# Kernel tuning notes

Hardware: AMD Instinct MI355X
Metric: run time of the kernel (lower is better)

The kernel has to match this reference:

```python
import jax, jax.numpy as jnp
import numpy as np

NUM_QUANTIZERS = 8
CODEBOOK_SIZE = 1024
DIM = 64
B, N = 8, 8192


def setup_inputs() -> dict:
    key = jax.random.key(0)
    kx, kc = jax.random.split(key)
    x = jax.random.normal(kx, (B, N, DIM), dtype=jnp.float32)
    # one codebook per quantizer stage (shared_codebook=False)
    codebooks = jax.random.normal(kc, (NUM_QUANTIZERS, CODEBOOK_SIZE, DIM), dtype=jnp.float32)
    return {"x": x, "codebooks": codebooks}


def reference(x, codebooks):
    """Residual VQ: sequential nearest-codebook lookup with residual subtraction.

    x:         [b, n, d]
    codebooks: [Q, K, d]
    returns quantized_out: [b, n, d]
    """

    def step(carry, cb):
        residual, qout = carry                       # [b,n,d], [b,n,d]
        # squared euclidean distances, [b,n,K]
        r_sq = jnp.sum(residual * residual, axis=-1, keepdims=True)
        c_sq = jnp.sum(cb * cb, axis=-1)             # [K]
        dots = jnp.einsum('bnd,kd->bnk', residual, cb)
        dist = r_sq - 2.0 * dots + c_sq              # [b,n,K]
        idx = jnp.argmin(dist, axis=-1)              # [b,n]
        quant = cb[idx]                              # [b,n,d] gather
        # straight-through estimator (VectorQuantize forward)
        quant_st = residual + jax.lax.stop_gradient(quant - residual)
        new_residual = residual - jax.lax.stop_gradient(quant)
        return (new_residual, qout + quant_st), idx

    init = (x, jnp.zeros_like(x))
    (residual, quantized_out), all_indices = jax.lax.scan(step, init, codebooks)
    return quantized_out
```

## Files before the change

### kernel.cpp

```cpp
#include <hip/hip_runtime.h>

#define NQ 8
#define KCODES 1024
#define D 64
#define CHUNK 64
#define NCHUNK 16
#define TPB 256
#define TOKPB 64
#define BIAS 96.0f

using short8 = __attribute__((ext_vector_type(8))) short;
using f32x4  = __attribute__((ext_vector_type(4))) float;

#define GLOBAL_AS __attribute__((address_space(1)))
#define LDS_AS    __attribute__((address_space(3)))

static __device__ __forceinline__ unsigned bf16_rne_bits(float f) {
    unsigned u = __float_as_uint(f);
    return (u + 0x7fffu + ((u >> 16) & 1u)) >> 16;
}
static __device__ __forceinline__ unsigned umn(unsigned a, unsigned b) { return a < b ? a : b; }
static __device__ __forceinline__ unsigned umx(unsigned a, unsigned b) { return a > b ? a : b; }
static __device__ __forceinline__ unsigned umed3(unsigned a, unsigned b, unsigned c) {
    return umx(umn(a, b), umn(umx(a, b), c));
}

__global__ __launch_bounds__(256) void prep_cb(const float* __restrict__ cb,
                                               int4* __restrict__ ws_cb) {
    int id = blockIdx.x * 256 + threadIdx.x;
    int n_rel = id & 63;
    int plane = (id >> 6) & 15;
    int ch    = (id >> 10) & 15;
    int q     = id >> 14;
    int g = plane & 3, kt = (plane >> 2) & 1, term = plane >> 3;
    int n = ch * CHUNK + n_rel;
    const float* src = cb + ((size_t)(q * KCODES + n)) * D + kt * 32 + g * 8;
    union { short s[8]; int4 v; } u;
    #pragma unroll
    for (int j = 0; j < 8; ++j) {
        float f = -src[j];
        unsigned hb = bf16_rne_bits(f);
        if (term == 0) {
            u.s[j] = (short)hb;
        } else {
            float lo = f - __uint_as_float(hb << 16);
            u.s[j] = (short)bf16_rne_bits(lo);
        }
    }
    ws_cb[id] = u.v;
}

__global__ __launch_bounds__(256) void prep_csq(const float* __restrict__ cb,
                                                float* __restrict__ ws_csq,
                                                float* __restrict__ ws_csqh) {
    int id = blockIdx.x * 256 + threadIdx.x;
    const float* c = cb + (size_t)id * D;
    float s0 = 0.f, s1 = 0.f, s2 = 0.f, s3 = 0.f;
    #pragma unroll
    for (int j = 0; j < 16; ++j) {
        s0 = fmaf(c[4*j+0], c[4*j+0], s0);
        s1 = fmaf(c[4*j+1], c[4*j+1], s1);
        s2 = fmaf(c[4*j+2], c[4*j+2], s2);
        s3 = fmaf(c[4*j+3], c[4*j+3], s3);
    }
    float cs = (s0 + s1) + (s2 + s3);
    ws_csq[id]  = cs;
    ws_csqh[id] = 0.5f * cs + BIAS;
}

__global__ __launch_bounds__(TPB, 4) void rvq_mfma(
    const float* __restrict__ x,
    const float* __restrict__ cb,
    const int4* __restrict__ ws_cb,
    const float* __restrict__ ws_csq,
    float* __restrict__ out)
{
    __shared__ __align__(16) int4  lds_stage[1024];
    __shared__ __align__(16) float lds_resid[TOKPB * 68];
    __shared__ float    lds_csqh[CHUNK];
    __shared__ unsigned lds_cand[2][TOKPB * 3];
    __shared__ int      lds_pick[TOKPB];

    const int tid   = threadIdx.x;
    const int lane  = tid & 63;
    const int wave  = tid >> 6;
    const int group = wave >> 1;
    const int half  = wave & 1;
    const int g     = lane >> 4;
    const int c     = lane & 15;
    const int tok0  = blockIdx.x * TOKPB;

    {
        const int t = tid >> 2, part = tid & 3;
        const float4* xp = (const float4*)(x + (size_t)(tok0 + t) * D + part * 16);
        float4* rr = (float4*)(lds_resid + t * 68 + part * 16);
        #pragma unroll
        for (int k2 = 0; k2 < 4; ++k2) rr[k2] = xp[k2];
    }

    const char* bp = (const char*)lds_stage + (c << 4) + (g << 10) + half * 512;

    for (int q = 0; q < NQ; ++q) {
        __syncthreads();

        short8 ah0[2], ah1[2], al0[2], al1[2];
        #pragma unroll
        for (int s = 0; s < 2; ++s) {
            const float* rr = lds_resid + (group * 32 + s * 16 + c) * 68;
            float4 f0 = *(const float4*)(rr + 8 * g);
            float4 f1 = *(const float4*)(rr + 8 * g + 4);
            float4 f2 = *(const float4*)(rr + 32 + 8 * g);
            float4 f3 = *(const float4*)(rr + 36 + 8 * g);
            const float* v0 = (const float*)&f0;
            const float* v1 = (const float*)&f1;
            const float* v2 = (const float*)&f2;
            const float* v3 = (const float*)&f3;
            #pragma unroll
            for (int j = 0; j < 4; ++j) {
                float a = v0[j], b = v1[j], e = v2[j], f = v3[j];
                unsigned ha = bf16_rne_bits(a);
                unsigned hb = bf16_rne_bits(b);
                unsigned he = bf16_rne_bits(e);
                unsigned hf = bf16_rne_bits(f);
                ah0[s][j]   = (short)ha;  ah0[s][4+j] = (short)hb;
                ah1[s][j]   = (short)he;  ah1[s][4+j] = (short)hf;
                al0[s][j]   = (short)bf16_rne_bits(a - __uint_as_float(ha << 16));
                al0[s][4+j] = (short)bf16_rne_bits(b - __uint_as_float(hb << 16));
                al1[s][j]   = (short)bf16_rne_bits(e - __uint_as_float(he << 16));
                al1[s][4+j] = (short)bf16_rne_bits(f - __uint_as_float(hf << 16));
            }
        }

        unsigned T1[2][4], T2[2][4], T3[2][4];
        #pragma unroll
        for (int s = 0; s < 2; ++s)
            #pragma unroll
            for (int r = 0; r < 4; ++r) { T1[s][r] = 0xFFFFFFFFu; T2[s][r] = 0xFFFFFFFFu; T3[s][r] = 0xFFFFFFFFu; }

        for (int ch = 0; ch < NCHUNK; ++ch) {
            __syncthreads();
            {
                const int4* src = ws_cb + (size_t)(q * NCHUNK + ch) * 1024 + tid;
                LDS_AS char* ldst = (LDS_AS char*)lds_stage + tid * 16;
                #pragma unroll
                for (int t = 0; t < 4; ++t) {
                    __builtin_amdgcn_global_load_lds(
                        (const GLOBAL_AS unsigned int*)(src + t * 256),
                        (LDS_AS unsigned int*)(ldst + t * 4096), 16, 0, 0);
                }
                if (tid < CHUNK) {
                    __builtin_amdgcn_global_load_lds(
                        (const GLOBAL_AS unsigned int*)(ws_csq + 8192 + q * KCODES + ch * CHUNK + tid),
                        (LDS_AS unsigned int*)(&lds_csqh[tid]), 4, 0, 0);
                }
            }
            __syncthreads();

            #pragma unroll
            for (int i = 0; i < 2; ++i) {
                short8 bh0 = *(const short8*)(bp + i * 256);
                short8 bh1 = *(const short8*)(bp + 4096  + i * 256);
                short8 bl0 = *(const short8*)(bp + 8192  + i * 256);
                short8 bl1 = *(const short8*)(bp + 12288 + i * 256);
                const float sd = lds_csqh[(half * 2 + i) * 16 + c];
                const unsigned codev = (unsigned)(ch * CHUNK + (half * 2 + i) * 16 + c);
                #pragma unroll
                for (int s = 0; s < 2; ++s) {
                    f32x4 acc = {sd, sd, sd, sd};
                    acc = __builtin_amdgcn_mfma_f32_16x16x32_bf16(ah0[s], bh0, acc, 0, 0, 0);
                    acc = __builtin_amdgcn_mfma_f32_16x16x32_bf16(ah1[s], bh1, acc, 0, 0, 0);
                    acc = __builtin_amdgcn_mfma_f32_16x16x32_bf16(al0[s], bh0, acc, 0, 0, 0);
                    acc = __builtin_amdgcn_mfma_f32_16x16x32_bf16(ah0[s], bl0, acc, 0, 0, 0);
                    acc = __builtin_amdgcn_mfma_f32_16x16x32_bf16(al1[s], bh1, acc, 0, 0, 0);
                    acc = __builtin_amdgcn_mfma_f32_16x16x32_bf16(ah1[s], bl1, acc, 0, 0, 0);
                    #pragma unroll
                    for (int r = 0; r < 4; ++r) {
                        unsigned p = (__float_as_uint(acc[r]) & 0xFFFFFC00u) | codev;
                        unsigned n2 = umn(T2[s][r], umx(T1[s][r], p));
                        unsigned n3 = umn(T3[s][r], umx(T2[s][r], p));
                        T1[s][r] = umn(T1[s][r], p);
                        T2[s][r] = n2;
                        T3[s][r] = n3;
                    }
                }
            }
        }

        #pragma unroll
        for (int st = 1; st <= 8; st <<= 1) {
            #pragma unroll
            for (int s = 0; s < 2; ++s) {
                #pragma unroll
                for (int r = 0; r < 4; ++r) {
                    unsigned o1 = (unsigned)__shfl_xor((int)T1[s][r], st);
                    unsigned o2 = (unsigned)__shfl_xor((int)T2[s][r], st);
                    unsigned o3 = (unsigned)__shfl_xor((int)T3[s][r], st);
                    unsigned x1 = umn(T1[s][r], o1), y1 = umx(T1[s][r], o1);
                    unsigned x2 = umn(T2[s][r], o2), y2 = umx(T2[s][r], o2);
                    unsigned x3 = umn(T3[s][r], o3);
                    T1[s][r] = x1;
                    T3[s][r] = umed3(y1, x2, umn(y2, x3));
                    T2[s][r] = umn(y1, x2);
                }
            }
        }

        if (c == 0) {
            #pragma unroll
            for (int s = 0; s < 2; ++s)
                #pragma unroll
                for (int r = 0; r < 4; ++r) {
                    const int idx = (group * 32 + s * 16 + g * 4 + r) * 3;
                    lds_cand[half][idx + 0] = T1[s][r];
                    lds_cand[half][idx + 1] = T2[s][r];
                    lds_cand[half][idx + 2] = T3[s][r];
                }
        }
        __syncthreads();

        {
            const int t4  = lane >> 2;
            const int sel = lane & 3;
            const int row = group * 32 + half * 16 + t4;
            unsigned a1 = lds_cand[0][row * 3 + 0];
            unsigned a2 = lds_cand[0][row * 3 + 1];
            unsigned a3 = lds_cand[0][row * 3 + 2];
            unsigned b1 = lds_cand[1][row * 3 + 0];
            unsigned b2 = lds_cand[1][row * 3 + 1];
            unsigned b3 = lds_cand[1][row * 3 + 2];
            unsigned x1 = umn(a1, b1), y1 = umx(a1, b1);
            unsigned x2 = umn(a2, b2), y2 = umx(a2, b2);
            unsigned x3 = umn(a3, b3);
            unsigned m1 = x1;
            unsigned m2 = umn(y1, x2);
            unsigned m3 = umed3(y1, x2, umn(y2, x3));
            const unsigned psel = (sel == 0) ? m1 : ((sel == 1) ? m2 : m3);
            const int cd = (int)(psel & 1023u);

            const float4* rrv = (const float4*)(lds_resid + row * 68);
            const float4* cpv = (const float4*)(cb + ((size_t)(q * KCODES + cd)) * D);
            float ax = 0.f, ay = 0.f, az = 0.f, aw = 0.f;
            #pragma unroll
            for (int j = 0; j < 16; ++j) {
                float4 rv = rrv[j];
                float4 cv = cpv[j];
                ax = fmaf(rv.x, cv.x, ax);
                ay = fmaf(rv.y, cv.y, ay);
                az = fmaf(rv.z, cv.z, az);
                aw = fmaf(rv.w, cv.w, aw);
            }
            float dot = (ax + ay) + (az + aw);
            float dd = fmaf(dot, -2.0f, ws_csq[q * KCODES + cd]);

            const int base = lane & ~3;
            float d0 = __shfl(dd, base);
            float d1 = __shfl(dd, base + 1);
            float d2 = __shfl(dd, base + 2);
            int cc0 = (int)(m1 & 1023u);
            int cc1 = (int)(m2 & 1023u);
            int cc2 = (int)(m3 & 1023u);
            float db = d0; int pick = cc0;
            if (d1 < db || (d1 == db && cc1 < pick)) { db = d1; pick = cc1; }
            if (d2 < db || (d2 == db && cc2 < pick)) { db = d2; pick = cc2; }
            if (sel == 0) lds_pick[row] = pick;
        }
        __syncthreads();

        {
            const int t = tid >> 2, part = tid & 3;
            const int ifin = lds_pick[t];
            const float4* cp = (const float4*)(cb + ((size_t)(q * KCODES + ifin)) * D + part * 16);
            float4* rr = (float4*)(lds_resid + t * 68 + part * 16);
            #pragma unroll
            for (int k2 = 0; k2 < 4; ++k2) {
                float4 rv = rr[k2], cv = cp[k2];
                rv.x -= cv.x; rv.y -= cv.y; rv.z -= cv.z; rv.w -= cv.w;
                rr[k2] = rv;
            }
        }
    }

    __syncthreads();
    {
        const int t = tid >> 2, part = tid & 3;
        const float4* xp = (const float4*)(x + (size_t)(tok0 + t) * D + part * 16);
        const float4* rr = (const float4*)(lds_resid + t * 68 + part * 16);
        float4* op = (float4*)(out + (size_t)(tok0 + t) * D + part * 16);
        #pragma unroll
        for (int k2 = 0; k2 < 4; ++k2) {
            float4 xv = xp[k2], rv = rr[k2];
            float4 o;
            o.x = xv.x - rv.x; o.y = xv.y - rv.y;
            o.z = xv.z - rv.z; o.w = xv.w - rv.w;
            op[k2] = o;
        }
    }
}

extern "C" void kernel_launch(void* const* d_in, const int* in_sizes, int n_in,
                              void* d_out, int out_size, void* d_ws, size_t ws_size,
                              hipStream_t stream) {
    const float* x  = (const float*)d_in[0];
    const float* cb = (const float*)d_in[1];
    float* out = (float*)d_out;

    int4*  ws_cb   = (int4*)d_ws;
    float* ws_csq  = (float*)((char*)d_ws + (size_t)2 * 1024 * 1024);
    float* ws_csqh = ws_csq + 8192;

    prep_cb <<<512, 256, 0, stream>>>(cb, ws_cb);
    prep_csq<<< 32, 256, 0, stream>>>(cb, ws_csq, ws_csqh);

    const int n_tokens = in_sizes[0] / D;
    const int grid = n_tokens / TOKPB;
    rvq_mfma<<<grid, TPB, 0, stream>>>(x, cb, ws_cb, ws_csq, out);
}
```

Before: 352.2 us.

## Double-buffer codebook chunk staging and double the tokens per block

Codebook chunk loads into LDS are now double-buffered. The next chunk's async global-to-LDS copy is issued before computing on the current buffer, which removes one barrier per chunk and overlaps the load with the MFMA and top-3 work. The squared-norm biases are packed into the same staging buffer. The block grows to 512 threads and 128 tokens, so each staged chunk is reused by twice as many tokens. The cost is twice the staging LDS and lower per-SM occupancy (launch bound 3).

```diff
diff --git a/kernel.cpp b/kernel.cpp
--- a/kernel.cpp
+++ b/kernel.cpp
@@ -5,9 +5,10 @@
 #define D 64
 #define CHUNK 64
 #define NCHUNK 16
-#define TPB 256
-#define TOKPB 64
+#define TPB 512
+#define TOKPB 128
 #define BIAS 96.0f
+#define STAGE_I4 1040
 
 using short8 = __attribute__((ext_vector_type(8))) short;
 using f32x4  = __attribute__((ext_vector_type(4))) float;
@@ -68,16 +69,15 @@
     ws_csqh[id] = 0.5f * cs + BIAS;
 }
 
-__global__ __launch_bounds__(TPB, 4) void rvq_mfma(
+__global__ __launch_bounds__(TPB, 3) void rvq_mfma(
     const float* __restrict__ x,
     const float* __restrict__ cb,
     const int4* __restrict__ ws_cb,
     const float* __restrict__ ws_csq,
     float* __restrict__ out)
 {
-    __shared__ __align__(16) int4  lds_stage[1024];
+    __shared__ __align__(16) int4  lds_stage[2][STAGE_I4];
     __shared__ __align__(16) float lds_resid[TOKPB * 68];
-    __shared__ float    lds_csqh[CHUNK];
     __shared__ unsigned lds_cand[2][TOKPB * 3];
     __shared__ int      lds_pick[TOKPB];
 
@@ -98,7 +98,24 @@
         for (int k2 = 0; k2 < 4; ++k2) rr[k2] = xp[k2];
     }
 
-    const char* bp = (const char*)lds_stage + (c << 4) + (g << 10) + half * 512;
+    const float* ws_csqh = ws_csq + 8192;
+    auto issue_chunk = [&](int step, int b) {
+        const int4* src = ws_cb + (size_t)step * 1024 + tid;
+        LDS_AS char* ldst = (LDS_AS char*)(&lds_stage[b][0]) + tid * 16;
+        __builtin_amdgcn_global_load_lds((const GLOBAL_AS unsigned int*)src,
+                                         (LDS_AS unsigned int*)ldst, 16, 0, 0);
+        __builtin_amdgcn_global_load_lds((const GLOBAL_AS unsigned int*)(src + 512),
+                                         (LDS_AS unsigned int*)(ldst + 512 * 16), 16, 0, 0);
+        if (tid < 16) {
+            const int4* cs = (const int4*)(ws_csqh + (size_t)step * 64) + tid;
+            LDS_AS unsigned* cdst =
+                (LDS_AS unsigned*)((LDS_AS char*)(&lds_stage[b][1024]) + tid * 16);
+            __builtin_amdgcn_global_load_lds((const GLOBAL_AS unsigned int*)cs, cdst, 16, 0, 0);
+        }
+    };
+
+    issue_chunk(0, 0);
+    int pbuf = 0;
 
     for (int q = 0; q < NQ; ++q) {
         __syncthreads();
@@ -139,22 +156,11 @@
 
         for (int ch = 0; ch < NCHUNK; ++ch) {
             __syncthreads();
-            {
-                const int4* src = ws_cb + (size_t)(q * NCHUNK + ch) * 1024 + tid;
-                LDS_AS char* ldst = (LDS_AS char*)lds_stage + tid * 16;
-                #pragma unroll
-                for (int t = 0; t < 4; ++t) {
-                    __builtin_amdgcn_global_load_lds(
-                        (const GLOBAL_AS unsigned int*)(src + t * 256),
-                        (LDS_AS unsigned int*)(ldst + t * 4096), 16, 0, 0);
-                }
-                if (tid < CHUNK) {
-                    __builtin_amdgcn_global_load_lds(
-                        (const GLOBAL_AS unsigned int*)(ws_csq + 8192 + q * KCODES + ch * CHUNK + tid),
-                        (LDS_AS unsigned int*)(&lds_csqh[tid]), 4, 0, 0);
-                }
-            }
-            __syncthreads();
+            const int nstep = q * NCHUNK + ch + 1;
+            if (nstep < NQ * NCHUNK) issue_chunk(nstep, pbuf ^ 1);
+
+            const char*  bp   = (const char*)&lds_stage[pbuf][0] + (c << 4) + (g << 10) + half * 512;
+            const float* csqb = (const float*)&lds_stage[pbuf][1024];
 
             #pragma unroll
             for (int i = 0; i < 2; ++i) {
@@ -162,7 +168,7 @@
                 short8 bh1 = *(const short8*)(bp + 4096  + i * 256);
                 short8 bl0 = *(const short8*)(bp + 8192  + i * 256);
                 short8 bl1 = *(const short8*)(bp + 12288 + i * 256);
-                const float sd = lds_csqh[(half * 2 + i) * 16 + c];
+                const float sd = csqb[(half * 2 + i) * 16 + c];
                 const unsigned codev = (unsigned)(ch * CHUNK + (half * 2 + i) * 16 + c);
                 #pragma unroll
                 for (int s = 0; s < 2; ++s) {
@@ -184,6 +190,7 @@
                     }
                 }
             }
+            pbuf ^= 1;
         }
 
         #pragma unroll
```

Result: slower. 488.6 us (+38.7%).
